# Kernel optimization log

Hardware: AMD Instinct MI355X
Metric: run time of the kernel (lower is better)

Reference implementation:

```python
import jax, jax.numpy as jnp
import numpy as np

N, V, C_IN, C_OUT = 8, 2048, 32, 64
ORDER, SUPPORT_LEN = 2, 3
BN_EPS = 1e-5


def _make_adj(key):
    a = jax.random.uniform(key, (N, V, V), dtype=jnp.float32)
    # row-normalize like a diffusion transition matrix
    return a / jnp.sum(a, axis=-1, keepdims=True)


def setup_inputs() -> dict:
    key = jax.random.key(0)
    ks = jax.random.split(key, 6)
    x = jax.random.normal(ks[0], (N, V, C_IN), dtype=jnp.float32)
    A0 = _make_adj(ks[1])
    A1 = _make_adj(ks[2])
    A2 = _make_adj(ks[3])
    c_in_total = (ORDER * SUPPORT_LEN + 1) * C_IN  # 224
    W = jax.random.normal(ks[4], (C_OUT, c_in_total), dtype=jnp.float32) / np.sqrt(c_in_total)
    b = jnp.zeros((C_OUT,), dtype=jnp.float32)
    gamma = jnp.ones((C_OUT,), dtype=jnp.float32)
    beta = jnp.zeros((C_OUT,), dtype=jnp.float32)
    return {"x": x, "A0": A0, "A1": A1, "A2": A2, "W": W, "b": b,
            "gamma": gamma, "beta": beta}


def reference(x, A0, A1, A2, W, b, gamma, beta):
    # nconv: einsum('nvl,nvw->nwl')
    nconv = lambda h, a: jnp.einsum('nvl,nvw->nwl', h, a)
    out = [x]
    for a in (A0, A1, A2):
        x1 = nconv(x, a)
        out.append(x1)
        for _ in range(2, ORDER + 1):
            x2 = nconv(x1, a)
            out.append(x2)
            x1 = x2
    h = jnp.concatenate(out, axis=-1)            # [N, V, 7*C_IN]
    # 1x1 Conv1d over channel axis == pointwise matmul + bias
    h = jnp.einsum('nvc,oc->nvo', h, W) + b      # [N, V, C_OUT]
    # BatchNorm1d (training-mode batch stats over batch and node dims)
    mean = jnp.mean(h, axis=(0, 1))
    var = jnp.var(h, axis=(0, 1))
    h = (h - mean) * jax.lax.rsqrt(var + BN_EPS) * gamma + beta
    # dropout p=0.0 -> identity
    return h
```

## Files before the change

kernel.cpp:

```cpp
#include <hip/hip_runtime.h>
#include <hip/hip_bf16.h>


#define V    2048
#define NB   8
#define CIN  32
#define COUT 64
#define CTOT 224

typedef __attribute__((ext_vector_type(8))) short bf16x8;
typedef __attribute__((ext_vector_type(16))) float f32x16;

static __device__ __forceinline__ short f2bf(float f) {
  __hip_bfloat16 h = __float2bfloat16(f);
  return *reinterpret_cast<short*>(&h);
}

static __device__ __forceinline__ void gll16(const float* g, float* l) {
  __builtin_amdgcn_global_load_lds(
      (const __attribute__((address_space(1))) void*)g,
      (__attribute__((address_space(3))) void*)l, 16, 0, 0);
}

__global__ __launch_bounds__(512, 4) void nconv_mfma_kernel(
    const float* __restrict__ Adj, const float* __restrict__ Xin,
    float* __restrict__ Xout) {
  __shared__ float SA[8][3][16][32];
  __shared__ float SX[8][2][16][32];

  const int bid  = blockIdx.x;
  const int n    = bid >> 6;
  const int ws   = (bid & 63) * 32;
  const int t    = threadIdx.x;
  const int wq   = t >> 6;
  const int lane = t & 63;
  const int g    = lane >> 5;
  const int mn   = lane & 31;

  const float* __restrict__ Asrc = Adj + (size_t)n * V * V +
                                   (size_t)(wq * 256) * V + ws +
                                   (size_t)(lane >> 3) * V + (lane & 7) * 4;
  const float* __restrict__ Xsrc =
      Xin + (size_t)n * V * CIN + wq * 256 * CIN + lane * 4;

  auto stage_a = [&](int slot, int c) {
    const float* a = Asrc + (size_t)c * (16 * V);
    gll16(a, &SA[wq][slot][0][0]);
    gll16(a + 8 * V, &SA[wq][slot][8][0]);
  };
  auto stage_x = [&](int slot, int c) {
    const float* x = Xsrc + c * (16 * CIN);
    gll16(x, &SX[wq][slot][0][0]);
    gll16(x + 256, &SX[wq][slot][8][0]);
  };

  f32x16 acc;
#pragma unroll
  for (int r = 0; r < 16; ++r) acc[r] = 0.f;

  auto compute = [&](int sa, int sx) {
    float a8[8], x8[8];
#pragma unroll
    for (int j = 0; j < 8; ++j) {
      a8[j] = SA[wq][sa][8 * g + j][mn];
      x8[j] = SX[wq][sx][8 * g + j][mn];
    }
    bf16x8 aop, bop;
#pragma unroll
    for (int j = 0; j < 8; ++j) {
      aop[j] = f2bf(x8[j]);
      bop[j] = f2bf(a8[j]);
    }
    acc = __builtin_amdgcn_mfma_f32_32x32x16_bf16(aop, bop, acc, 0, 0, 0);
  };

#define WAITV(N)                                          \
  do {                                                    \
    asm volatile("s_waitcnt vmcnt(" #N ")" ::: "memory"); \
    __builtin_amdgcn_sched_barrier(0);                    \
  } while (0)

  stage_a(0, 0);
  stage_x(0, 0);
  stage_a(1, 1);

  int ca = 0, cx = 0;
#pragma unroll 1
  for (int i = 0; i < 14; ++i) {
    stage_x(cx ^ 1, i + 1);
    const int as = (ca == 0) ? 2 : ca - 1;
    stage_a(as, i + 2);
    WAITV(6);
    compute(ca, cx);
    ca = (ca == 2) ? 0 : ca + 1;
    cx ^= 1;
  }
  stage_x(cx ^ 1, 15);
  WAITV(4);
  compute(ca, cx);
  ca = (ca == 2) ? 0 : ca + 1;
  cx ^= 1;
  WAITV(0);
  compute(ca, cx);

#undef WAITV

  __syncthreads();
  float(*Lred)[32][33] = reinterpret_cast<float(*)[32][33]>(&SA[0][0][0][0]);
#pragma unroll
  for (int r = 0; r < 16; ++r) {
    Lred[wq][(r & 3) + 8 * (r >> 2) + 4 * g][mn] = acc[r];
  }
  __syncthreads();
  const int w  = t >> 4;
  const int l0 = (t & 15) * 2;
  float2 o;
  o.x = 0.f;
  o.y = 0.f;
#pragma unroll
  for (int k = 0; k < 8; ++k) {
    o.x += Lred[k][l0][w];
    o.y += Lred[k][l0 + 1][w];
  }
  *(float2*)(Xout + ((size_t)n * V + ws + w) * CIN + l0) = o;
}

__global__ __launch_bounds__(256) void conv_bn_stats_kernel(
    const float* __restrict__ W, const float* __restrict__ bias,
    const float* __restrict__ p0, const float* __restrict__ p1,
    const float* __restrict__ p2, const float* __restrict__ p3,
    const float* __restrict__ p4, const float* __restrict__ p5,
    const float* __restrict__ p6, float* __restrict__ hout,
    float* __restrict__ stats) {
  __shared__ float Wl[COUT * CTOT];
  __shared__ float Fl[64 * CTOT];
  const int t = threadIdx.x;
  const int R0 = blockIdx.x * 64;

#pragma unroll
  for (int s = 0; s < 14; ++s) {
    int fl = t + s * 256;
    int o = fl / 56, c4 = fl % 56;
    float4 wv = *(const float4*)(W + o * CTOT + c4 * 4);
    int c = c4 * 4;
    int csw = c ^ (((o >> 2) & 7) << 2);
    *(float4*)&Wl[o * CTOT + csw] = wv;
  }
  const float* parts[7] = {p0, p1, p2, p3, p4, p5, p6};
#pragma unroll
  for (int p = 0; p < 7; ++p) {
    const float* __restrict__ src = parts[p] + (size_t)R0 * CIN;
#pragma unroll
    for (int s = 0; s < 2; ++s) {
      int fl = t + s * 256;
      int r = fl >> 3, c4 = fl & 7;
      float4 v = *(const float4*)(src + r * CIN + c4 * 4);
      int c = p * 32 + c4 * 4;
      int csw = c ^ (((r >> 2) & 7) << 2);
      *(float4*)&Fl[r * CTOT + csw] = v;
    }
  }
  __syncthreads();

  const int rg = t & 15, og = t >> 4;
  const int r0 = rg * 4, o0 = og * 4;
  float acc[4][4];
#pragma unroll
  for (int i = 0; i < 4; ++i)
#pragma unroll
    for (int j = 0; j < 4; ++j) acc[i][j] = bias[o0 + j];

  const int fsw = (rg & 7) << 2;
  const int wsw = (og & 7) << 2;
  for (int cc = 0; cc < CTOT; cc += 4) {
    float4 f[4], w[4];
#pragma unroll
    for (int i = 0; i < 4; ++i)
      f[i] = *(const float4*)&Fl[(r0 + i) * CTOT + (cc ^ fsw)];
#pragma unroll
    for (int j = 0; j < 4; ++j)
      w[j] = *(const float4*)&Wl[(o0 + j) * CTOT + (cc ^ wsw)];
#pragma unroll
    for (int i = 0; i < 4; ++i)
#pragma unroll
      for (int j = 0; j < 4; ++j)
        acc[i][j] += f[i].x * w[j].x + f[i].y * w[j].y + f[i].z * w[j].z +
                     f[i].w * w[j].w;
  }

#pragma unroll
  for (int i = 0; i < 4; ++i) {
    *(float4*)(hout + (size_t)(R0 + r0 + i) * COUT + o0) =
        make_float4(acc[i][0], acc[i][1], acc[i][2], acc[i][3]);
  }

  __syncthreads();
  float* red = Fl;
#pragma unroll
  for (int j = 0; j < 4; ++j) {
    float s = acc[0][j] + acc[1][j] + acc[2][j] + acc[3][j];
    float qq = acc[0][j] * acc[0][j] + acc[1][j] * acc[1][j] +
               acc[2][j] * acc[2][j] + acc[3][j] * acc[3][j];
    red[(o0 + j) * 16 + rg] = s;
    red[1024 + (o0 + j) * 16 + rg] = qq;
  }
  __syncthreads();
  if (t < 128) {
    int o = t & 63, which = t >> 6;
    const float* b = red + which * 1024 + o * 16;
    float v = 0.f;
#pragma unroll
    for (int k = 0; k < 16; ++k) v += b[k];
    atomicAdd(stats + which * COUT + o, v);
  }
}

__global__ __launch_bounds__(256) void bn_apply_kernel(
    float* __restrict__ hout, const float* __restrict__ stats,
    const float* __restrict__ gamma, const float* __restrict__ beta) {
  const int i4 = blockIdx.x * 256 + threadIdx.x;
  const int oi = i4 & 15;
  float4 h = ((const float4*)hout)[i4];
  const float4 s = ((const float4*)stats)[oi];
  const float4 q = ((const float4*)(stats + COUT))[oi];
  const float4 g = ((const float4*)gamma)[oi];
  const float4 bb = ((const float4*)beta)[oi];
  const float inv = 1.f / 16384.f;
  float m, vv, rs;
  m = s.x * inv; vv = q.x * inv - m * m; rs = rsqrtf(vv + 1e-5f);
  h.x = (h.x - m) * rs * g.x + bb.x;
  m = s.y * inv; vv = q.y * inv - m * m; rs = rsqrtf(vv + 1e-5f);
  h.y = (h.y - m) * rs * g.y + bb.y;
  m = s.z * inv; vv = q.z * inv - m * m; rs = rsqrtf(vv + 1e-5f);
  h.z = (h.z - m) * rs * g.z + bb.z;
  m = s.w * inv; vv = q.w * inv - m * m; rs = rsqrtf(vv + 1e-5f);
  h.w = (h.w - m) * rs * g.w + bb.w;
  ((float4*)hout)[i4] = h;
}

extern "C" void kernel_launch(void* const* d_in, const int* in_sizes, int n_in,
                              void* d_out, int out_size, void* d_ws,
                              size_t ws_size, hipStream_t stream) {
  const float* x     = (const float*)d_in[0];
  const float* A0    = (const float*)d_in[1];
  const float* A1    = (const float*)d_in[2];
  const float* A2    = (const float*)d_in[3];
  const float* W     = (const float*)d_in[4];
  const float* b     = (const float*)d_in[5];
  const float* gamma = (const float*)d_in[6];
  const float* beta  = (const float*)d_in[7];
  float* out = (float*)d_out;

  char* ws = (char*)d_ws;
  float* stats = (float*)ws;
  const size_t BUF = (size_t)NB * V * CIN;
  float* x1_0 = (float*)(ws + 4096);
  float* x2_0 = x1_0 + BUF;
  float* x1_1 = x2_0 + BUF;
  float* x2_1 = x1_1 + BUF;
  float* x1_2 = x2_1 + BUF;
  float* x2_2 = x1_2 + BUF;

  hipMemsetAsync(stats, 0, 2 * COUT * sizeof(float), stream);

  dim3 g(512), blk(512);
  nconv_mfma_kernel<<<g, blk, 0, stream>>>(A0, x, x1_0);
  nconv_mfma_kernel<<<g, blk, 0, stream>>>(A0, x1_0, x2_0);
  nconv_mfma_kernel<<<g, blk, 0, stream>>>(A1, x, x1_1);
  nconv_mfma_kernel<<<g, blk, 0, stream>>>(A1, x1_1, x2_1);
  nconv_mfma_kernel<<<g, blk, 0, stream>>>(A2, x, x1_2);
  nconv_mfma_kernel<<<g, blk, 0, stream>>>(A2, x1_2, x2_2);

  conv_bn_stats_kernel<<<dim3(256), dim3(256), 0, stream>>>(
      W, b, x, x1_0, x2_0, x1_1, x2_1, x1_2, x2_2, out, stats);
  bn_apply_kernel<<<dim3(1024), dim3(256), 0, stream>>>(out, stats, gamma,
                                                        beta);
}
```

Measured before the change: 212.2 us.

## Fuse six nconv launches into one persistent kernel reusing adjacency fragments in registers

Merges the six per-support diffusion kernels into a single persistent kernel that runs all three supports. For each support it computes the first hop, then does a grid-wide atomic-counter barrier, then computes the second hop. The bf16 adjacency fragments loaded for the first hop are kept in registers, so the second hop reads only the intermediate features and never reads the large adjacency matrix again. This roughly halves adjacency traffic and removes launch overhead. In exchange it adds grid-sync spins, needs all 512 blocks co-resident, and raises register pressure from holding 16 fragments.

```diff
diff --git a/kernel.cpp b/kernel.cpp
--- a/kernel.cpp
+++ b/kernel.cpp
@@ -22,107 +22,182 @@
       (__attribute__((address_space(3))) void*)l, 16, 0, 0);
 }
 
-__global__ __launch_bounds__(512, 4) void nconv_mfma_kernel(
-    const float* __restrict__ Adj, const float* __restrict__ Xin,
-    float* __restrict__ Xout) {
+__global__ __launch_bounds__(512, 4) void gcn_chain_kernel(
+    const float* __restrict__ A0g, const float* __restrict__ A1g,
+    const float* __restrict__ A2g, const float* __restrict__ Xg,
+    float* __restrict__ x1a, float* __restrict__ x2a,
+    float* __restrict__ x1b, float* __restrict__ x2b,
+    float* __restrict__ x1c, float* __restrict__ x2c,
+    unsigned* __restrict__ cnt) {
   __shared__ float SA[8][3][16][32];
   __shared__ float SX[8][2][16][32];
 
   const int bid  = blockIdx.x;
   const int n    = bid >> 6;
-  const int ws   = (bid & 63) * 32;
+  const int wcol = (bid & 63) * 32;
   const int t    = threadIdx.x;
   const int wq   = t >> 6;
   const int lane = t & 63;
   const int g    = lane >> 5;
   const int mn   = lane & 31;
 
-  const float* __restrict__ Asrc = Adj + (size_t)n * V * V +
-                                   (size_t)(wq * 256) * V + ws +
-                                   (size_t)(lane >> 3) * V + (lane & 7) * 4;
   const float* __restrict__ Xsrc =
-      Xin + (size_t)n * V * CIN + wq * 256 * CIN + lane * 4;
-
-  auto stage_a = [&](int slot, int c) {
-    const float* a = Asrc + (size_t)c * (16 * V);
-    gll16(a, &SA[wq][slot][0][0]);
-    gll16(a + 8 * V, &SA[wq][slot][8][0]);
+      Xg + (size_t)n * V * CIN + wq * 256 * CIN + lane * 4;
+
+  f32x16 acc;
+
+  auto reduce_store = [&](float* __restrict__ Out) {
+    __syncthreads();
+    float(*Lred)[32][33] = reinterpret_cast<float(*)[32][33]>(&SA[0][0][0][0]);
+#pragma unroll
+    for (int r = 0; r < 16; ++r)
+      Lred[wq][(r & 3) + 8 * (r >> 2) + 4 * g][mn] = acc[r];
+    __syncthreads();
+    const int w  = t >> 4;
+    const int l0 = (t & 15) * 2;
+    float2 o;
+    o.x = 0.f;
+    o.y = 0.f;
+#pragma unroll
+    for (int k = 0; k < 8; ++k) {
+      o.x += Lred[k][l0][w];
+      o.y += Lred[k][l0 + 1][w];
+    }
+    *(float2*)(Out + ((size_t)n * V + wcol + w) * CIN + l0) = o;
+    __syncthreads();
   };
-  auto stage_x = [&](int slot, int c) {
-    const float* x = Xsrc + c * (16 * CIN);
-    gll16(x, &SX[wq][slot][0][0]);
-    gll16(x + 256, &SX[wq][slot][8][0]);
+
+  auto grid_sync = [&](unsigned target) {
+    __threadfence();
+    __syncthreads();
+    if (t == 0) {
+      __hip_atomic_fetch_add(cnt, 1u, __ATOMIC_RELEASE,
+                             __HIP_MEMORY_SCOPE_AGENT);
+      while (__hip_atomic_load(cnt, __ATOMIC_ACQUIRE,
+                               __HIP_MEMORY_SCOPE_AGENT) < target)
+        __builtin_amdgcn_s_sleep(32);
+    }
+    __syncthreads();
+    __threadfence();
   };
 
-  f32x16 acc;
-#pragma unroll
-  for (int r = 0; r < 16; ++r) acc[r] = 0.f;
-
-  auto compute = [&](int sa, int sx) {
-    float a8[8], x8[8];
-#pragma unroll
-    for (int j = 0; j < 8; ++j) {
-      a8[j] = SA[wq][sa][8 * g + j][mn];
-      x8[j] = SX[wq][sx][8 * g + j][mn];
-    }
-    bf16x8 aop, bop;
-#pragma unroll
-    for (int j = 0; j < 8; ++j) {
-      aop[j] = f2bf(x8[j]);
-      bop[j] = f2bf(a8[j]);
-    }
-    acc = __builtin_amdgcn_mfma_f32_32x32x16_bf16(aop, bop, acc, 0, 0, 0);
-  };
-
-#define WAITV(N)                                          \
+#define WV(N)                                             \
   do {                                                    \
     asm volatile("s_waitcnt vmcnt(" #N ")" ::: "memory"); \
     __builtin_amdgcn_sched_barrier(0);                    \
   } while (0)
 
-  stage_a(0, 0);
-  stage_x(0, 0);
-  stage_a(1, 1);
-
-  int ca = 0, cx = 0;
+#define STGA(SL, C)                                          \
+  do {                                                       \
+    const float* a_ = Apl + (size_t)(C) * (16 * V);          \
+    gll16(a_, &SA[wq][SL][0][0]);                            \
+    gll16(a_ + (size_t)8 * V, &SA[wq][SL][8][0]);            \
+  } while (0)
+
+#define STGX(SL, C)                                          \
+  do {                                                       \
+    const float* x_ = Xsrc + (C) * (16 * CIN);               \
+    gll16(x_, &SX[wq][SL][0][0]);                            \
+    gll16(x_ + 256, &SX[wq][SL][8][0]);                      \
+  } while (0)
+
+#define STGY(SL, C)                                          \
+  do {                                                       \
+    const float* y_ = Yp + (C) * (16 * CIN);                 \
+    gll16(y_, &SX[wq][SL][0][0]);                            \
+    gll16(y_ + 256, &SX[wq][SL][8][0]);                      \
+  } while (0)
+
+#define CMPA(ASL, XSL, C)                                                 \
+  do {                                                                    \
+    float a8[8], x8[8];                                                   \
+    _Pragma("unroll") for (int j = 0; j < 8; ++j) {                       \
+      a8[j] = SA[wq][ASL][8 * g + j][mn];                                 \
+      x8[j] = SX[wq][XSL][8 * g + j][mn];                                 \
+    }                                                                     \
+    bf16x8 aop_;                                                          \
+    _Pragma("unroll") for (int j = 0; j < 8; ++j) {                       \
+      aop_[j]   = f2bf(x8[j]);                                            \
+      bfr[C][j] = f2bf(a8[j]);                                            \
+    }                                                                     \
+    acc = __builtin_amdgcn_mfma_f32_32x32x16_bf16(aop_, bfr[C], acc,      \
+                                                  0, 0, 0);               \
+  } while (0)
+
+#define CMPB(XSL, C)                                                      \
+  do {                                                                    \
+    float y8[8];                                                          \
+    _Pragma("unroll") for (int j = 0; j < 8; ++j)                         \
+      y8[j] = SX[wq][XSL][8 * g + j][mn];                                 \
+    bf16x8 aop_;                                                          \
+    _Pragma("unroll") for (int j = 0; j < 8; ++j) aop_[j] = f2bf(y8[j]);  \
+    acc = __builtin_amdgcn_mfma_f32_32x32x16_bf16(aop_, bfr[C], acc,      \
+                                                  0, 0, 0);               \
+  } while (0)
+
 #pragma unroll 1
-  for (int i = 0; i < 14; ++i) {
-    stage_x(cx ^ 1, i + 1);
-    const int as = (ca == 0) ? 2 : ca - 1;
-    stage_a(as, i + 2);
-    WAITV(6);
-    compute(ca, cx);
-    ca = (ca == 2) ? 0 : ca + 1;
-    cx ^= 1;
-  }
-  stage_x(cx ^ 1, 15);
-  WAITV(4);
-  compute(ca, cx);
-  ca = (ca == 2) ? 0 : ca + 1;
-  cx ^= 1;
-  WAITV(0);
-  compute(ca, cx);
-
-#undef WAITV
-
-  __syncthreads();
-  float(*Lred)[32][33] = reinterpret_cast<float(*)[32][33]>(&SA[0][0][0][0]);
-#pragma unroll
-  for (int r = 0; r < 16; ++r) {
-    Lred[wq][(r & 3) + 8 * (r >> 2) + 4 * g][mn] = acc[r];
-  }
-  __syncthreads();
-  const int w  = t >> 4;
-  const int l0 = (t & 15) * 2;
-  float2 o;
-  o.x = 0.f;
-  o.y = 0.f;
-#pragma unroll
-  for (int k = 0; k < 8; ++k) {
-    o.x += Lred[k][l0][w];
-    o.y += Lred[k][l0 + 1][w];
-  }
-  *(float2*)(Xout + ((size_t)n * V + ws + w) * CIN + l0) = o;
+  for (int ch = 0; ch < 3; ++ch) {
+    const float* __restrict__ Adj = ch == 0 ? A0g : (ch == 1 ? A1g : A2g);
+    float* __restrict__ X1 = ch == 0 ? x1a : (ch == 1 ? x1b : x1c);
+    float* __restrict__ X2 = ch == 0 ? x2a : (ch == 1 ? x2b : x2c);
+    const float* __restrict__ Apl =
+        Adj + (size_t)n * V * V + (size_t)(wq * 256) * V + wcol +
+        (size_t)(lane >> 3) * V + (lane & 7) * 4;
+
+    bf16x8 bfr[16];
+
+#pragma unroll
+    for (int r = 0; r < 16; ++r) acc[r] = 0.f;
+    STGA(0, 0); STGX(0, 0); STGA(1, 1);
+    STGX(1, 1);  STGA(2, 2);  WV(6); CMPA(0, 0, 0);
+    STGX(0, 2);  STGA(0, 3);  WV(6); CMPA(1, 1, 1);
+    STGX(1, 3);  STGA(1, 4);  WV(6); CMPA(2, 0, 2);
+    STGX(0, 4);  STGA(2, 5);  WV(6); CMPA(0, 1, 3);
+    STGX(1, 5);  STGA(0, 6);  WV(6); CMPA(1, 0, 4);
+    STGX(0, 6);  STGA(1, 7);  WV(6); CMPA(2, 1, 5);
+    STGX(1, 7);  STGA(2, 8);  WV(6); CMPA(0, 0, 6);
+    STGX(0, 8);  STGA(0, 9);  WV(6); CMPA(1, 1, 7);
+    STGX(1, 9);  STGA(1, 10); WV(6); CMPA(2, 0, 8);
+    STGX(0, 10); STGA(2, 11); WV(6); CMPA(0, 1, 9);
+    STGX(1, 11); STGA(0, 12); WV(6); CMPA(1, 0, 10);
+    STGX(0, 12); STGA(1, 13); WV(6); CMPA(2, 1, 11);
+    STGX(1, 13); STGA(2, 14); WV(6); CMPA(0, 0, 12);
+    STGX(0, 14); STGA(0, 15); WV(6); CMPA(1, 1, 13);
+    STGX(1, 15);              WV(4); CMPA(2, 0, 14);
+                              WV(0); CMPA(0, 1, 15);
+    reduce_store(X1);
+    grid_sync(512u * (unsigned)(ch + 1));
+
+    const float* __restrict__ Yp =
+        X1 + (size_t)n * V * CIN + wq * 256 * CIN + lane * 4;
+#pragma unroll
+    for (int r = 0; r < 16; ++r) acc[r] = 0.f;
+    STGY(0, 0);
+    STGY(1, 1);  WV(2); CMPB(0, 0);
+    STGY(0, 2);  WV(2); CMPB(1, 1);
+    STGY(1, 3);  WV(2); CMPB(0, 2);
+    STGY(0, 4);  WV(2); CMPB(1, 3);
+    STGY(1, 5);  WV(2); CMPB(0, 4);
+    STGY(0, 6);  WV(2); CMPB(1, 5);
+    STGY(1, 7);  WV(2); CMPB(0, 6);
+    STGY(0, 8);  WV(2); CMPB(1, 7);
+    STGY(1, 9);  WV(2); CMPB(0, 8);
+    STGY(0, 10); WV(2); CMPB(1, 9);
+    STGY(1, 11); WV(2); CMPB(0, 10);
+    STGY(0, 12); WV(2); CMPB(1, 11);
+    STGY(1, 13); WV(2); CMPB(0, 12);
+    STGY(0, 14); WV(2); CMPB(1, 13);
+    STGY(1, 15); WV(2); CMPB(0, 14);
+                 WV(0); CMPB(1, 15);
+    reduce_store(X2);
+  }
+
+#undef WV
+#undef STGA
+#undef STGX
+#undef STGY
+#undef CMPA
+#undef CMPB
 }
 
 __global__ __launch_bounds__(256) void conv_bn_stats_kernel(
@@ -253,6 +328,7 @@
 
   char* ws = (char*)d_ws;
   float* stats = (float*)ws;
+  unsigned* cnt = (unsigned*)(ws + 2048);
   const size_t BUF = (size_t)NB * V * CIN;
   float* x1_0 = (float*)(ws + 4096);
   float* x2_0 = x1_0 + BUF;
@@ -261,15 +337,10 @@
   float* x1_2 = x2_1 + BUF;
   float* x2_2 = x1_2 + BUF;
 
-  hipMemsetAsync(stats, 0, 2 * COUT * sizeof(float), stream);
-
-  dim3 g(512), blk(512);
-  nconv_mfma_kernel<<<g, blk, 0, stream>>>(A0, x, x1_0);
-  nconv_mfma_kernel<<<g, blk, 0, stream>>>(A0, x1_0, x2_0);
-  nconv_mfma_kernel<<<g, blk, 0, stream>>>(A1, x, x1_1);
-  nconv_mfma_kernel<<<g, blk, 0, stream>>>(A1, x1_1, x2_1);
-  nconv_mfma_kernel<<<g, blk, 0, stream>>>(A2, x, x1_2);
-  nconv_mfma_kernel<<<g, blk, 0, stream>>>(A2, x1_2, x2_2);
+  hipMemsetAsync(ws, 0, 4096, stream);
+
+  gcn_chain_kernel<<<dim3(512), dim3(512), 0, stream>>>(
+      A0, A1, A2, x, x1_0, x2_0, x1_1, x2_1, x1_2, x2_2, cnt);
 
   conv_bn_stats_kernel<<<dim3(256), dim3(256), 0, stream>>>(
       W, b, x, x1_0, x2_0, x1_1, x2_1, x1_2, x2_2, out, stats);
```

After: 838.7 us. +295.2%, slower.
